# Kernel tuning notes

Measured on AMD Instinct MI355X. Metric: run time of the kernel, lower is better.

The kernel has to match this reference:

```python
import jax, jax.numpy as jnp
import numpy as np
from jax import lax

EPS = 1e-5  # BatchNorm eps (torch default)

def _up2_bilinear_ac(x):
    # bilinear upsample x2, align_corners=True; x: [B,C,H,W]
    B, C, H, W = x.shape
    def axis_interp(n_in, n_out):
        pos = jnp.arange(n_out, dtype=jnp.float32) * ((n_in - 1) / (n_out - 1))
        i0 = jnp.floor(pos).astype(jnp.int32)
        i1 = jnp.minimum(i0 + 1, n_in - 1)
        w = (pos - i0.astype(jnp.float32)).astype(x.dtype)
        return i0, i1, w
    i0, i1, wh = axis_interp(H, 2 * H)
    x = x[:, :, i0, :] * (1.0 - wh)[None, None, :, None] + x[:, :, i1, :] * wh[None, None, :, None]
    j0, j1, ww = axis_interp(W, 2 * W)
    x = x[:, :, :, j0] * (1.0 - ww) + x[:, :, :, j1] * ww
    return x

def setup_inputs() -> dict:
    key = jax.random.key(0)
    ks = jax.random.split(key, 8)
    B, Cin, Cout, H, W = 8, 64, 32, 128, 128
    att, K = 16, 2  # attention_channel = max(int(64*0.0625),16)=16; kernel_num=2
    n = lambda k, s, sc: jax.random.normal(k, s, jnp.float32) * sc
    return {
        'x': n(ks[0], (B, Cin, H, W), 1.0),
        'fc_w': n(ks[1], (att, Cin), 0.1),
        'bn_a_gamma': jnp.ones((att,), jnp.float32), 'bn_a_beta': jnp.zeros((att,), jnp.float32),
        'bn_a_mean': jnp.zeros((att,), jnp.float32), 'bn_a_var': jnp.ones((att,), jnp.float32),
        'ch_w': n(ks[2], (Cin, att), 0.1), 'ch_b': jnp.zeros((Cin,), jnp.float32),
        'fil_w': n(ks[3], (Cout, att), 0.1), 'fil_b': jnp.zeros((Cout,), jnp.float32),
        'sp_w': n(ks[4], (9, att), 0.1), 'sp_b': jnp.zeros((9,), jnp.float32),
        'k_w': n(ks[5], (K, att), 0.1), 'k_b': jnp.zeros((K,), jnp.float32),
        'weight': n(ks[6], (K, Cout, Cin, 3, 3), 0.05),
        'bn_gamma': jnp.ones((Cout,), jnp.float32), 'bn_beta': jnp.zeros((Cout,), jnp.float32),
        'bn_mean': jnp.zeros((Cout,), jnp.float32), 'bn_var': jnp.ones((Cout,), jnp.float32),
    }

def reference(x, fc_w, bn_a_gamma, bn_a_beta, bn_a_mean, bn_a_var,
              ch_w, ch_b, fil_w, fil_b, sp_w, sp_b, k_w, k_b,
              weight, bn_gamma, bn_beta, bn_mean, bn_var):
    x = _up2_bilinear_ac(x)
    B, Cin, H, W = x.shape
    K, Cout = weight.shape[0], weight.shape[1]
    # --- ODConv attention branch (on GAP features) ---
    g = x.mean(axis=(2, 3))                                    # [B,Cin]
    h = g @ fc_w.T                                             # [B,att]
    h = (h - bn_a_mean) / jnp.sqrt(bn_a_var + EPS) * bn_a_gamma + bn_a_beta
    h = jax.nn.relu(h)
    ch_att = jax.nn.sigmoid(h @ ch_w.T + ch_b)                 # [B,Cin]
    fil_att = jax.nn.sigmoid(h @ fil_w.T + fil_b)              # [B,Cout]
    sp_att = jax.nn.sigmoid(h @ sp_w.T + sp_b).reshape(B, 1, 1, 1, 3, 3)
    k_att = jax.nn.softmax(h @ k_w.T + k_b, axis=1).reshape(B, K, 1, 1, 1, 1)
    # per-sample aggregated filters: [B,Cout,Cin,3,3]
    agg_w = jnp.sum(k_att * sp_att * weight[None], axis=1)
    # --- dynamic conv (per-sample filter), channel-attended input ---
    x = x * ch_att[:, :, None, None]
    def conv1(xi, wi):
        return lax.conv_general_dilated(xi[None], wi, (1, 1), [(1, 1), (1, 1)],
                                        dimension_numbers=('NCHW', 'OIHW', 'NCHW'))[0]
    y = jax.vmap(conv1)(x, agg_w)                              # [B,Cout,H,W]
    y = y * fil_att[:, :, None, None]
    # --- BatchNorm2d (inference) + GELU (exact erf) ---
    y = (y - bn_mean[:, None, None]) / jnp.sqrt(bn_var[:, None, None] + EPS)
    y = y * bn_gamma[:, None, None] + bn_beta[:, None, None]
    return jax.nn.gelu(y, approximate=False)
```

## Files before the change

kernel.cpp:

```cpp
#include <hip/hip_runtime.h>
#include <hip/hip_bf16.h>

#define EPSBN 1e-5f

typedef short short8 __attribute__((ext_vector_type(8)));
typedef float f32x16 __attribute__((ext_vector_type(16)));

static __device__ __forceinline__ unsigned short f2u(float f){
  __hip_bfloat16 h = __float2bfloat16(f);
  union { __hip_bfloat16 h; unsigned short u; } c; c.h = h; return c.u;
}

#define WS_G     2048
#define WS_S     7168
#define WS_T     8192
#define WS_AGGB  16384
#define WS_XUP   327680

__global__ __launch_bounds__(256) void k_up(const float* __restrict__ x,
                                            unsigned int* __restrict__ xup32,
                                            float* __restrict__ g)
{
  __shared__ float xin[16*798];
  __shared__ float w[128];
  int tid = threadIdx.x;
  int bi  = blockIdx.x;
  int strip = bi & 31, h16 = (bi >> 5) & 3, b = bi >> 7;
  int r0 = strip * 8;
  int i0b = (int)((float)r0 * (127.0f/255.0f));

  if (tid < 128){
    int i = tid;
    float s = 0.f;
    int rstart = max(0, (int)floorf((float)(i-1)*(255.0f/127.0f)));
    #pragma unroll
    for (int k = 0; k < 8; ++k){
      int r = rstart + k;
      if (r <= 255){
        float pos = (float)r * (127.0f/255.0f);
        int i0 = (int)pos; float fr = pos - (float)i0; int i1 = min(i0+1,127);
        if (i0 == i) s += 1.0f - fr;
        if (i1 == i) s += fr;
      }
    }
    w[i] = s;
  }
  for (int e = tid; e < 12288; e += 256){
    int ir = e >> 11, rem = e & 2047, ci = rem >> 7, j = rem & 127;
    int row = min(i0b + ir, 127);
    xin[ci*798 + ir*133 + j] = x[(((size_t)(b*64 + h16*16 + ci)) << 14) + (row << 7) + j];
  }
  __syncthreads();

  {
    int ci_l = tid >> 4, kk = tid & 15;
    float s = 0.f;
    const float* base = &xin[ci_l*798];
    #pragma unroll
    for (int row = 0; row < 4; ++row){
      int grow = 4*strip + row;
      int ir = grow - i0b;
      const float* rp = base + ir*133 + kk*8;
      float ss = 0.f;
      #pragma unroll
      for (int j = 0; j < 8; ++j) ss += rp[j]*w[kk*8+j];
      s += w[grow]*ss;
    }
    s += __shfl_down(s, 8, 16);
    s += __shfl_down(s, 4, 16);
    s += __shfl_down(s, 2, 16);
    s += __shfl_down(s, 1, 16);
    if (kk == 0) atomicAdd(&g[b*64 + h16*16 + ci_l], s*(1.0f/65536.0f));
  }

  int ci2 = tid & 7, cbase = tid >> 3;
  int j0t[8], j1t[8]; float wwt[8];
  #pragma unroll
  for (int jj = 0; jj < 8; ++jj){
    int c = cbase + 32*jj;
    float pos = (float)c * (127.0f/255.0f);
    int j0 = (int)pos;
    j0t[jj] = j0; j1t[jj] = min(j0+1,127); wwt[jj] = pos - (float)j0;
  }
  const float* base0 = &xin[(ci2*2+0)*798];
  const float* base1 = &xin[(ci2*2+1)*798];
  size_t plane32 = ((size_t)(b*4 + h16)) << 19;

  for (int rr = 0; rr < 8; ++rr){
    int r = r0 + rr;
    float posr = (float)r * (127.0f/255.0f);
    int i0 = (int)posr; float wh = posr - (float)i0;
    int ir0 = (i0 - i0b)*133, ir1 = (min(i0+1,127) - i0b)*133;
    #pragma unroll
    for (int jj = 0; jj < 8; ++jj){
      int c = cbase + 32*jj;
      int j0 = j0t[jj], j1 = j1t[jj]; float ww = wwt[jj];
      float v00 = base0[ir0+j0], v01 = base0[ir0+j1];
      float v10 = base0[ir1+j0], v11 = base0[ir1+j1];
      float a0 = v00 + (v01-v00)*ww;
      float a1 = v10 + (v11-v10)*ww;
      float r0v = a0 + (a1-a0)*wh;
      float u00 = base1[ir0+j0], u01 = base1[ir0+j1];
      float u10 = base1[ir1+j0], u11 = base1[ir1+j1];
      float b0 = u00 + (u01-u00)*ww;
      float b1 = u10 + (u11-u10)*ww;
      float r1v = b0 + (b1-b0)*wh;
      unsigned pack = (unsigned)f2u(r0v) | (((unsigned)f2u(r1v)) << 16);
      xup32[plane32 + (size_t)(r*256 + c)*8 + ci2] = pack;
    }
  }
}

__global__ __launch_bounds__(256) void k_aggw(const float* __restrict__ g,
                      const float* __restrict__ fc_w,
                      const float* __restrict__ bga, const float* __restrict__ bba,
                      const float* __restrict__ bma, const float* __restrict__ bva,
                      const float* __restrict__ ch_w, const float* __restrict__ ch_b,
                      const float* __restrict__ fil_w, const float* __restrict__ fil_b,
                      const float* __restrict__ sp_w, const float* __restrict__ sp_b,
                      const float* __restrict__ k_w, const float* __restrict__ k_b,
                      const float* __restrict__ bn_g, const float* __restrict__ bn_b,
                      const float* __restrict__ bn_m, const float* __restrict__ bn_v,
                      const float* __restrict__ weight,
                      unsigned short* __restrict__ aggb,
                      float* __restrict__ sS, float* __restrict__ tT)
{
  __shared__ float h[8][16];
  int tid = threadIdx.x;
  if (tid < 128){
    int b = tid >> 4, a = tid & 15;
    float acc = 0.f;
    for (int c = 0; c < 64; ++c) acc += g[b*64+c] * fc_w[a*64+c];
    float v = (acc - bma[a]) * rsqrtf(bva[a] + EPSBN) * bga[a] + bba[a];
    h[b][a] = fmaxf(v, 0.f);
  }
  __syncthreads();

  int idx = blockIdx.x*256 + tid;
  int ci_l = idx & 31;
  int o    = (idx >> 5) & 31;
  int s    = (idx >> 10) % 9;
  int t2   = (idx >> 10) / 9;
  int cc   = t2 & 1, b = t2 >> 1;
  int ci   = cc*32 + ci_l;

  const float* hb = h[b];
  float zc = ch_b[ci], zs = sp_b[s];
  float z0 = k_b[0],  z1 = k_b[1];
  #pragma unroll
  for (int a = 0; a < 16; ++a){
    float hv = hb[a];
    zc += hv*ch_w[ci*16+a];
    zs += hv*sp_w[s*16+a];
    z0 += hv*k_w[a];
    z1 += hv*k_w[16+a];
  }
  float chv = 1.f/(1.f+expf(-zc));
  float spv = 1.f/(1.f+expf(-zs));
  float m = fmaxf(z0,z1);
  float e0 = expf(z0-m), e1 = expf(z1-m), inv = 1.f/(e0+e1);
  float ka0 = e0*inv, ka1 = e1*inv;
  float w0 = weight[(o*64+ci)*9+s];
  float w1 = weight[((32+o)*64+ci)*9+s];
  aggb[idx] = f2u(chv*spv*(ka0*w0 + ka1*w1));

  if (blockIdx.x == 0){
    int bb = tid >> 5, oo = tid & 31;
    float z = fil_b[oo];
    #pragma unroll
    for (int a = 0; a < 16; ++a) z += h[bb][a]*fil_w[oo*16+a];
    float f = 1.f/(1.f+expf(-z));
    float invs = rsqrtf(bn_v[oo] + EPSBN);
    sS[tid] = f * bn_g[oo] * invs;
    if (bb == 0) tT[oo] = bn_b[oo] - bn_m[oo]*bn_g[oo]*invs;
  }
}

#define XT_STRIDE 40

static __device__ __forceinline__ void xdesc(int e, int p0, int q0,
                                             int& ldso, int& pmo, bool& v){
  int rr = e / 72; int rem = e - rr*72;
  int qq = rem >> 2; int k2 = (rem >> 1) & 1; int kqe = rem & 1;
  int gr = p0 - 1 + rr, gq = q0 - 1 + qq;
  v    = ((unsigned)gr < 256u) && ((unsigned)gq < 256u);
  ldso = (rr*18+qq)*XT_STRIDE + k2*16 + kqe*8;
  pmo  = (k2 << 20) + (gr*256+gq)*16 + kqe*8;
}

__global__ __launch_bounds__(256) void k_conv(const unsigned short* __restrict__ xup,
                                              const unsigned short* __restrict__ aggb,
                                              const float* __restrict__ sS,
                                              const float* __restrict__ tT,
                                              float* __restrict__ out)
{
  __shared__ unsigned short xt[18*18*XT_STRIDE];
  __shared__ float sSs[32], tTs[32];

  int tid = threadIdx.x;
  int bi  = blockIdx.x;
  int b   = bi >> 8, t = bi & 255;
  int p0  = (t >> 4) * 16, q0 = (t & 15) * 16;
  int lane = tid & 63, wv = tid >> 6;
  if (tid < 32){ sSs[tid] = sS[b*32+tid]; tTs[tid] = tT[tid]; }

  f32x16 acc[2];
  #pragma unroll
  for (int i = 0; i < 16; ++i){ acc[0][i] = 0.f; acc[1][i] = 0.f; }

  int n  = lane & 31;
  int kq = lane >> 5;
  int lr0 = 2*(2*wv + 0) + (n >> 4);
  int lr1 = 2*(2*wv + 1) + (n >> 4);
  int qb  = n & 15;

  const unsigned short* xb0 = xup + (((size_t)(b*4 + 0)) << 20);
  const unsigned short* xb1 = xup + (((size_t)(b*4 + 2)) << 20);
  const short8 zero8 = {0,0,0,0,0,0,0,0};

  #pragma unroll
  for (int k = 0; k < 6; ++k){
    int e = tid + (k << 8); if (e >= 1296) e -= 1296;
    int ldso, pmo; bool v;
    xdesc(e, p0, q0, ldso, pmo, v);
    short8 vv = zero8;
    if (v) vv = *(const short8*)&xb0[pmo];
    *(short8*)&xt[ldso] = vv;
  }
  short8 pre[6];
  #pragma unroll
  for (int k = 0; k < 6; ++k){
    int e = tid + (k << 8); if (e >= 1296) e -= 1296;
    int ldso, pmo; bool v;
    xdesc(e, p0, q0, ldso, pmo, v);
    pre[k] = zero8;
    if (v) pre[k] = *(const short8*)&xb1[pmo];
  }
  __syncthreads();

  auto kloop = [&](const unsigned short* ab){
    short8 a0 = *(const short8*)&ab[0];
    short8 a1 = *(const short8*)&ab[16];
    #pragma unroll
    for (int s = 0; s < 9; ++s){
      int sn = (s < 8) ? s+1 : 8;
      short8 na0 = *(const short8*)&ab[sn*1024];
      short8 na1 = *(const short8*)&ab[sn*1024+16];
      const int ky = s/3, kx = s%3;
      {
        const unsigned short* xrow = &xt[((lr0+ky)*18 + qb+kx)*XT_STRIDE + kq*8];
        short8 bv0 = *(const short8*)&xrow[0];
        short8 bv1 = *(const short8*)&xrow[16];
        acc[0] = __builtin_amdgcn_mfma_f32_32x32x16_bf16(a0, bv0, acc[0], 0, 0, 0);
        acc[0] = __builtin_amdgcn_mfma_f32_32x32x16_bf16(a1, bv1, acc[0], 0, 0, 0);
      }
      {
        const unsigned short* xrow = &xt[((lr1+ky)*18 + qb+kx)*XT_STRIDE + kq*8];
        short8 bv0 = *(const short8*)&xrow[0];
        short8 bv1 = *(const short8*)&xrow[16];
        acc[1] = __builtin_amdgcn_mfma_f32_32x32x16_bf16(a0, bv0, acc[1], 0, 0, 0);
        acc[1] = __builtin_amdgcn_mfma_f32_32x32x16_bf16(a1, bv1, acc[1], 0, 0, 0);
      }
      a0 = na0; a1 = na1;
    }
  };

  kloop(aggb + (size_t)(b*2+0)*9216 + n*32 + kq*8);
  __syncthreads();
  #pragma unroll
  for (int k = 0; k < 6; ++k){
    int e = tid + (k << 8); if (e >= 1296) e -= 1296;
    int ldso, pmo; bool v;
    xdesc(e, p0, q0, ldso, pmo, v);
    *(short8*)&xt[ldso] = pre[k];
  }
  __syncthreads();
  kloop(aggb + (size_t)(b*2+1)*9216 + n*32 + kq*8);

  #pragma unroll
  for (int tt = 0; tt < 2; ++tt){
    int lr = (tt == 0) ? lr0 : lr1;
    int p = p0 + lr, q = q0 + qb;
    #pragma unroll
    for (int r = 0; r < 16; ++r){
      int o = (r & 3) + 8*(r >> 2) + 4*kq;
      float valv = acc[tt][r]*sSs[o] + tTs[o];
      float gl  = 0.5f*valv*(1.f + erff(valv*0.70710678118f));
      out[(((size_t)(b*32+o)) << 16) + (p << 8) + q] = gl;
    }
  }
}

extern "C" void kernel_launch(void* const* d_in, const int* in_sizes, int n_in,
                              void* d_out, int out_size, void* d_ws, size_t ws_size,
                              hipStream_t stream)
{
  const float* x     = (const float*)d_in[0];
  const float* fc_w  = (const float*)d_in[1];
  const float* bga   = (const float*)d_in[2];
  const float* bba   = (const float*)d_in[3];
  const float* bma   = (const float*)d_in[4];
  const float* bva   = (const float*)d_in[5];
  const float* ch_w  = (const float*)d_in[6];
  const float* ch_b  = (const float*)d_in[7];
  const float* fil_w = (const float*)d_in[8];
  const float* fil_b = (const float*)d_in[9];
  const float* sp_w  = (const float*)d_in[10];
  const float* sp_b  = (const float*)d_in[11];
  const float* k_w   = (const float*)d_in[12];
  const float* k_b   = (const float*)d_in[13];
  const float* weight= (const float*)d_in[14];
  const float* bn_g  = (const float*)d_in[15];
  const float* bn_b  = (const float*)d_in[16];
  const float* bn_m  = (const float*)d_in[17];
  const float* bn_v  = (const float*)d_in[18];

  char* ws = (char*)d_ws;
  float* g   = (float*)(ws + WS_G);
  float* sS  = (float*)(ws + WS_S);
  float* tT  = (float*)(ws + WS_T);
  unsigned short* aggb = (unsigned short*)(ws + WS_AGGB);
  unsigned short* xup  = (unsigned short*)(ws + WS_XUP);
  float* out = (float*)d_out;

  hipMemsetAsync(g, 0, 512*sizeof(float), stream);
  hipLaunchKernelGGL(k_up,   dim3(1024), dim3(256), 0, stream, x, (unsigned int*)xup, g);
  hipLaunchKernelGGL(k_aggw, dim3(576),  dim3(256), 0, stream, g, fc_w, bga, bba, bma, bva,
                     ch_w, ch_b, fil_w, fil_b, sp_w, sp_b, k_w, k_b,
                     bn_g, bn_b, bn_m, bn_v, weight, aggb, sS, tT);
  hipLaunchKernelGGL(k_conv, dim3(2048), dim3(256), 0, stream, xup, aggb, sS, tT, out);
}
```

Baseline: 193.0 us.

## Widen conv tiles to 16x32, vectorize upsample loads, reuse row interpolants

The conv kernel now computes a 16x32 output tile per block with four accumulators per wave. This halves the block count, amortizes the halo overhead and the per-block filter loads, and adds a batch-interleaved block swizzle. The upsample kernel loads input rows with float4 into a padded shared buffer and walks output rows per column, reusing horizontally interpolated rows instead of reloading four taps per output. The costs are more registers (four accumulators plus ten prefetch vectors) and a larger LDS footprint, which may lower occupancy.

```diff
diff --git a/kernel.cpp b/kernel.cpp
--- a/kernel.cpp
+++ b/kernel.cpp
@@ -17,11 +17,13 @@
 #define WS_AGGB  16384
 #define WS_XUP   327680
 
+#define XIN_S 820
+
 __global__ __launch_bounds__(256) void k_up(const float* __restrict__ x,
                                             unsigned int* __restrict__ xup32,
                                             float* __restrict__ g)
 {
-  __shared__ float xin[16*798];
+  __shared__ float xin[16*XIN_S];
   __shared__ float w[128];
   int tid = threadIdx.x;
   int bi  = blockIdx.x;
@@ -45,22 +47,28 @@
     }
     w[i] = s;
   }
-  for (int e = tid; e < 12288; e += 256){
-    int ir = e >> 11, rem = e & 2047, ci = rem >> 7, j = rem & 127;
+  for (int e4 = tid; e4 < 3072; e4 += 256){
+    int j4 = e4 & 31, ci = (e4 >> 5) & 15, ir = e4 >> 9;
     int row = min(i0b + ir, 127);
-    xin[ci*798 + ir*133 + j] = x[(((size_t)(b*64 + h16*16 + ci)) << 14) + (row << 7) + j];
+    *(float4*)&xin[ci*XIN_S + ir*136 + j4*4] =
+      *(const float4*)&x[(((size_t)(b*64 + h16*16 + ci)) << 14) + (row << 7) + j4*4];
+  }
+  for (int e2 = tid; e2 < 768; e2 += 256){
+    int k = e2 & 7, t8 = e2 >> 3;
+    int ir = t8 % 6, ci = t8 / 6;
+    xin[ci*XIN_S + ir*136 + 128 + k] = 0.f;
   }
   __syncthreads();
 
   {
     int ci_l = tid >> 4, kk = tid & 15;
     float s = 0.f;
-    const float* base = &xin[ci_l*798];
+    const float* base = &xin[ci_l*XIN_S];
     #pragma unroll
     for (int row = 0; row < 4; ++row){
       int grow = 4*strip + row;
       int ir = grow - i0b;
-      const float* rp = base + ir*133 + kk*8;
+      const float* rp = base + ir*136 + kk*8;
       float ss = 0.f;
       #pragma unroll
       for (int j = 0; j < 8; ++j) ss += rp[j]*w[kk*8+j];
@@ -74,37 +82,39 @@
   }
 
   int ci2 = tid & 7, cbase = tid >> 3;
-  int j0t[8], j1t[8]; float wwt[8];
+  const float* b0p = &xin[(ci2*2+0)*XIN_S];
+  const float* b1p = &xin[(ci2*2+1)*XIN_S];
+  size_t plane32 = ((size_t)(b*4 + h16)) << 19;
+
   #pragma unroll
   for (int jj = 0; jj < 8; ++jj){
     int c = cbase + 32*jj;
     float pos = (float)c * (127.0f/255.0f);
-    int j0 = (int)pos;
-    j0t[jj] = j0; j1t[jj] = min(j0+1,127); wwt[jj] = pos - (float)j0;
-  }
-  const float* base0 = &xin[(ci2*2+0)*798];
-  const float* base1 = &xin[(ci2*2+1)*798];
-  size_t plane32 = ((size_t)(b*4 + h16)) << 19;
-
-  for (int rr = 0; rr < 8; ++rr){
-    int r = r0 + rr;
-    float posr = (float)r * (127.0f/255.0f);
-    int i0 = (int)posr; float wh = posr - (float)i0;
-    int ir0 = (i0 - i0b)*133, ir1 = (min(i0+1,127) - i0b)*133;
-    #pragma unroll
-    for (int jj = 0; jj < 8; ++jj){
-      int c = cbase + 32*jj;
-      int j0 = j0t[jj], j1 = j1t[jj]; float ww = wwt[jj];
-      float v00 = base0[ir0+j0], v01 = base0[ir0+j1];
-      float v10 = base0[ir1+j0], v11 = base0[ir1+j1];
-      float a0 = v00 + (v01-v00)*ww;
-      float a1 = v10 + (v11-v10)*ww;
-      float r0v = a0 + (a1-a0)*wh;
-      float u00 = base1[ir0+j0], u01 = base1[ir0+j1];
-      float u10 = base1[ir1+j0], u11 = base1[ir1+j1];
-      float b0 = u00 + (u01-u00)*ww;
-      float b1 = u10 + (u11-u10)*ww;
-      float r1v = b0 + (b1-b0)*wh;
+    int j0 = (int)pos; float ww = pos - (float)j0;
+
+    int irA = 0;
+    float A0, B0, A1, B1;
+    {
+      float x0 = b0p[j0],     x1 = b0p[j0+1];     A0 = x0 + (x1-x0)*ww;
+      float y0 = b1p[j0],     y1 = b1p[j0+1];     A1 = y0 + (y1-y0)*ww;
+      float x2 = b0p[136+j0], x3 = b0p[136+j0+1]; B0 = x2 + (x3-x2)*ww;
+      float y2 = b1p[136+j0], y3 = b1p[136+j0+1]; B1 = y2 + (y3-y2)*ww;
+    }
+    #pragma unroll
+    for (int rr = 0; rr < 8; ++rr){
+      int r = r0 + rr;
+      float posr = (float)r * (127.0f/255.0f);
+      int i0 = (int)posr; float wh = posr - (float)i0;
+      int ir0 = i0 - i0b;
+      if (ir0 > irA){
+        A0 = B0; A1 = B1;
+        int irB = ir0 + 1;
+        float x0 = b0p[irB*136+j0], x1 = b0p[irB*136+j0+1]; B0 = x0 + (x1-x0)*ww;
+        float y0 = b1p[irB*136+j0], y1 = b1p[irB*136+j0+1]; B1 = y0 + (y1-y0)*ww;
+        irA = ir0;
+      }
+      float r0v = A0 + (B0-A0)*wh;
+      float r1v = A1 + (B1-A1)*wh;
       unsigned pack = (unsigned)f2u(r0v) | (((unsigned)f2u(r1v)) << 16);
       xup32[plane32 + (size_t)(r*256 + c)*8 + ci2] = pack;
     }
@@ -178,63 +188,50 @@
 
 #define XT_STRIDE 40
 
-static __device__ __forceinline__ void xdesc(int e, int p0, int q0,
-                                             int& ldso, int& pmo, bool& v){
-  int rr = e / 72; int rem = e - rr*72;
-  int qq = rem >> 2; int k2 = (rem >> 1) & 1; int kqe = rem & 1;
-  int gr = p0 - 1 + rr, gq = q0 - 1 + qq;
-  v    = ((unsigned)gr < 256u) && ((unsigned)gq < 256u);
-  ldso = (rr*18+qq)*XT_STRIDE + k2*16 + kqe*8;
-  pmo  = (k2 << 20) + (gr*256+gq)*16 + kqe*8;
-}
-
 __global__ __launch_bounds__(256) void k_conv(const unsigned short* __restrict__ xup,
                                               const unsigned short* __restrict__ aggb,
                                               const float* __restrict__ sS,
                                               const float* __restrict__ tT,
                                               float* __restrict__ out)
 {
-  __shared__ unsigned short xt[18*18*XT_STRIDE];
+  __shared__ unsigned short xt[18*34*XT_STRIDE];
   __shared__ float sSs[32], tTs[32];
 
   int tid = threadIdx.x;
   int bi  = blockIdx.x;
-  int b   = bi >> 8, t = bi & 255;
-  int p0  = (t >> 4) * 16, q0 = (t & 15) * 16;
+  int sw  = ((bi & 7) << 7) + (bi >> 3);
+  int b   = sw >> 7, t = sw & 127;
+  int p0  = (t >> 3) * 16, q0 = (t & 7) * 32;
   int lane = tid & 63, wv = tid >> 6;
   if (tid < 32){ sSs[tid] = sS[b*32+tid]; tTs[tid] = tT[tid]; }
 
-  f32x16 acc[2];
-  #pragma unroll
-  for (int i = 0; i < 16; ++i){ acc[0][i] = 0.f; acc[1][i] = 0.f; }
-
-  int n  = lane & 31;
-  int kq = lane >> 5;
-  int lr0 = 2*(2*wv + 0) + (n >> 4);
-  int lr1 = 2*(2*wv + 1) + (n >> 4);
-  int qb  = n & 15;
+  f32x16 acc[4];
+  #pragma unroll
+  for (int i = 0; i < 16; ++i){ acc[0][i]=0.f; acc[1][i]=0.f; acc[2][i]=0.f; acc[3][i]=0.f; }
+
+  int n     = lane & 31;
+  int kq    = lane >> 5;
+  int rhalf = n >> 4;
+  int qb    = n & 15;
+  int wrow  = wv * 4;
 
   const unsigned short* xb0 = xup + (((size_t)(b*4 + 0)) << 20);
   const unsigned short* xb1 = xup + (((size_t)(b*4 + 2)) << 20);
   const short8 zero8 = {0,0,0,0,0,0,0,0};
 
-  #pragma unroll
-  for (int k = 0; k < 6; ++k){
-    int e = tid + (k << 8); if (e >= 1296) e -= 1296;
-    int ldso, pmo; bool v;
-    xdesc(e, p0, q0, ldso, pmo, v);
-    short8 vv = zero8;
-    if (v) vv = *(const short8*)&xb0[pmo];
-    *(short8*)&xt[ldso] = vv;
-  }
-  short8 pre[6];
-  #pragma unroll
-  for (int k = 0; k < 6; ++k){
-    int e = tid + (k << 8); if (e >= 1296) e -= 1296;
-    int ldso, pmo; bool v;
-    xdesc(e, p0, q0, ldso, pmo, v);
-    pre[k] = zero8;
-    if (v) pre[k] = *(const short8*)&xb1[pmo];
+  short8 pre[10];
+  #pragma unroll
+  for (int k = 0; k < 10; ++k){
+    int e = tid + (k << 8); if (e >= 2448) e -= 2448;
+    int rr = e / 136, rem = e - rr*136;
+    int qq = rem >> 2, k2 = (rem >> 1) & 1, kqe = rem & 1;
+    int gr = p0 - 1 + rr, gq = q0 - 1 + qq;
+    bool v = ((unsigned)gr < 256u) && ((unsigned)gq < 256u);
+    int ldso = (rr*34 + qq)*XT_STRIDE + k2*16 + kqe*8;
+    int pmo  = (k2 << 20) + (gr*256 + gq)*16 + kqe*8;
+    short8 cur = zero8; pre[k] = zero8;
+    if (v){ cur = *(const short8*)&xb0[pmo]; pre[k] = *(const short8*)&xb1[pmo]; }
+    *(short8*)&xt[ldso] = cur;
   }
   __syncthreads();
 
@@ -247,19 +244,15 @@
       short8 na0 = *(const short8*)&ab[sn*1024];
       short8 na1 = *(const short8*)&ab[sn*1024+16];
       const int ky = s/3, kx = s%3;
-      {
-        const unsigned short* xrow = &xt[((lr0+ky)*18 + qb+kx)*XT_STRIDE + kq*8];
+      #pragma unroll
+      for (int tt = 0; tt < 4; ++tt){
+        const int rp = tt >> 1, cb = tt & 1;
+        const unsigned short* xrow =
+          &xt[((wrow + 2*rp + rhalf + ky)*34 + cb*16 + qb + kx)*XT_STRIDE + kq*8];
         short8 bv0 = *(const short8*)&xrow[0];
         short8 bv1 = *(const short8*)&xrow[16];
-        acc[0] = __builtin_amdgcn_mfma_f32_32x32x16_bf16(a0, bv0, acc[0], 0, 0, 0);
-        acc[0] = __builtin_amdgcn_mfma_f32_32x32x16_bf16(a1, bv1, acc[0], 0, 0, 0);
-      }
-      {
-        const unsigned short* xrow = &xt[((lr1+ky)*18 + qb+kx)*XT_STRIDE + kq*8];
-        short8 bv0 = *(const short8*)&xrow[0];
-        short8 bv1 = *(const short8*)&xrow[16];
-        acc[1] = __builtin_amdgcn_mfma_f32_32x32x16_bf16(a0, bv0, acc[1], 0, 0, 0);
-        acc[1] = __builtin_amdgcn_mfma_f32_32x32x16_bf16(a1, bv1, acc[1], 0, 0, 0);
+        acc[tt] = __builtin_amdgcn_mfma_f32_32x32x16_bf16(a0, bv0, acc[tt], 0, 0, 0);
+        acc[tt] = __builtin_amdgcn_mfma_f32_32x32x16_bf16(a1, bv1, acc[tt], 0, 0, 0);
       }
       a0 = na0; a1 = na1;
     }
@@ -268,19 +261,21 @@
   kloop(aggb + (size_t)(b*2+0)*9216 + n*32 + kq*8);
   __syncthreads();
   #pragma unroll
-  for (int k = 0; k < 6; ++k){
-    int e = tid + (k << 8); if (e >= 1296) e -= 1296;
-    int ldso, pmo; bool v;
-    xdesc(e, p0, q0, ldso, pmo, v);
+  for (int k = 0; k < 10; ++k){
+    int e = tid + (k << 8); if (e >= 2448) e -= 2448;
+    int rr = e / 136, rem = e - rr*136;
+    int qq = rem >> 2, k2 = (rem >> 1) & 1, kqe = rem & 1;
+    int ldso = (rr*34 + qq)*XT_STRIDE + k2*16 + kqe*8;
     *(short8*)&xt[ldso] = pre[k];
   }
   __syncthreads();
   kloop(aggb + (size_t)(b*2+1)*9216 + n*32 + kq*8);
 
   #pragma unroll
-  for (int tt = 0; tt < 2; ++tt){
-    int lr = (tt == 0) ? lr0 : lr1;
-    int p = p0 + lr, q = q0 + qb;
+  for (int tt = 0; tt < 4; ++tt){
+    int rp = tt >> 1, cb = tt & 1;
+    int p = p0 + wrow + 2*rp + rhalf;
+    int q = q0 + cb*16 + qb;
     #pragma unroll
     for (int r = 0; r < 16; ++r){
       int o = (r & 3) + 8*(r >> 2) + 4*kq;
@@ -328,5 +323,5 @@
   hipLaunchKernelGGL(k_aggw, dim3(576),  dim3(256), 0, stream, g, fc_w, bga, bba, bma, bva,
                      ch_w, ch_b, fil_w, fil_b, sp_w, sp_b, k_w, k_b,
                      bn_g, bn_b, bn_m, bn_v, weight, aggb, sS, tT);
-  hipLaunchKernelGGL(k_conv, dim3(2048), dim3(256), 0, stream, xup, aggb, sS, tT, out);
-}
+  hipLaunchKernelGGL(k_conv, dim3(1024), dim3(256), 0, stream, xup, aggb, sS, tT, out);
+}
```

After: 182.2 us. -5.6%, faster.
